# Optimization experiments

Measured on AMD Instinct MI355X. Metric: run time of the kernel, lower is better.

## Reference

```python
import jax, jax.numpy as jnp
import numpy as np


def _gcn(A, x, W, b):
    # GCNConv(improved=True): add_remaining_self_loops(fill=2), symmetric normalization.
    n = A.shape[0]
    idx = jnp.arange(n)
    d = jnp.diagonal(A)
    Ahat = A.at[idx, idx].set(jnp.where(d == 0, 2.0, d))  # keep existing self-loop weights
    dinv = 1.0 / jnp.sqrt(Ahat.sum(axis=1))
    return (Ahat * dinv[:, None] * dinv[None, :]) @ (x @ W) + b


def _augment(A):
    # GraphUNet.augment_adj: add self loops, A @ A (spspmm), remove self loops.
    n = A.shape[0]
    idx = jnp.arange(n)
    A1 = A.at[idx, idx].add(1.0)
    return (A1 @ A1).at[idx, idx].set(0.0)


def _pool(A, x, p, k):
    # TopKPooling with tanh nonlinearity.
    score = jnp.tanh((x @ p) / jnp.linalg.norm(p))
    vals, perm = jax.lax.top_k(score, k)
    return A[perm][:, perm], x[perm] * vals[:, None], perm


def _gat(mask, x, W, a_src, a_dst, b, heads, c, concat):
    # GATConv, eval mode (attention dropout inactive). mask[dst, src] includes self loops.
    n = x.shape[0]
    h = (x @ W).reshape(n, heads, c)
    es = jnp.einsum('shc,hc->sh', h, a_src)
    ed = jnp.einsum('dhc,hc->dh', h, a_dst)
    logits = jax.nn.leaky_relu(ed[:, None, :] + es[None, :, :], 0.2)  # [dst, src, h]
    logits = jnp.where(mask[:, :, None], logits, jnp.finfo(logits.dtype).min)
    alpha = jax.nn.softmax(logits, axis=1)  # softmax over sources per destination
    out = jnp.einsum('dsh,shc->dhc', alpha, h)
    out = out.reshape(n, heads * c) if concat else out.mean(axis=1)
    return out + b


def setup_inputs() -> dict:
    key = jax.random.key(0)
    ks = jax.random.split(key, 34)
    N, E, IN, H, OUT, HEADS = 4096, 65536, 3, 64, 128, 4
    r = lambda k, s: jax.random.normal(k, s, jnp.float32) * 0.1
    inp = {}
    inp['x'] = jax.random.normal(ks[0], (N, IN), jnp.float32)
    inp['edge_index'] = jax.random.randint(ks[1], (2, E), 0, N)
    inp['unet_w0'] = r(ks[2], (IN, H)); inp['unet_b0'] = jnp.zeros((H,), jnp.float32)
    inp['unet_w1'] = r(ks[3], (H, H)); inp['unet_b1'] = jnp.zeros((H,), jnp.float32)
    inp['unet_w2'] = r(ks[4], (H, H)); inp['unet_b2'] = jnp.zeros((H,), jnp.float32)
    inp['unet_w3'] = r(ks[5], (H, H)); inp['unet_b3'] = jnp.zeros((H,), jnp.float32)
    inp['pool_p1'] = r(ks[6], (H,)); inp['pool_p2'] = r(ks[7], (H,)); inp['pool_p3'] = r(ks[8], (H,))
    inp['up_w0'] = r(ks[9], (H, H)); inp['up_b0'] = jnp.zeros((H,), jnp.float32)
    inp['up_w1'] = r(ks[10], (H, H)); inp['up_b1'] = jnp.zeros((H,), jnp.float32)
    inp['up_w2'] = r(ks[11], (H, OUT)); inp['up_b2'] = jnp.zeros((OUT,), jnp.float32)
    inp['ln_g'] = jnp.ones((OUT,), jnp.float32); inp['ln_b'] = jnp.zeros((OUT,), jnp.float32)
    inp['res_w'] = r(ks[12], (OUT, OUT)); inp['res_b'] = jnp.zeros((OUT,), jnp.float32)
    inp['gat1_w'] = r(ks[13], (OUT, HEADS * OUT))
    inp['gat1_asrc'] = r(ks[14], (HEADS, OUT)); inp['gat1_adst'] = r(ks[15], (HEADS, OUT))
    inp['gat1_b'] = jnp.zeros((HEADS * OUT,), jnp.float32)
    inp['gat2_w'] = r(ks[16], (HEADS * OUT, OUT))
    inp['gat2_asrc'] = r(ks[17], (1, OUT)); inp['gat2_adst'] = r(ks[18], (1, OUT))
    inp['gat2_b'] = jnp.zeros((OUT,), jnp.float32)
    return inp


def reference(x, edge_index, unet_w0, unet_b0, unet_w1, unet_b1, unet_w2, unet_b2,
              unet_w3, unet_b3, pool_p1, pool_p2, pool_p3, up_w0, up_b0, up_w1, up_b1,
              up_w2, up_b2, ln_g, ln_b, res_w, res_b, gat1_w, gat1_asrc, gat1_adst,
              gat1_b, gat2_w, gat2_asrc, gat2_adst, gat2_b):
    n0 = x.shape[0]
    # Dense weighted adjacency A[dst, src]; duplicate edges accumulate weight (scatter-add).
    A0 = jnp.zeros((n0, n0), x.dtype).at[edge_index[1], edge_index[0]].add(1.0)
    # ---- GraphUNet down path ----
    x0 = jax.nn.relu(_gcn(A0, x, unet_w0, unet_b0))
    k1 = (n0 + 1) // 2
    A1, h1, perm1 = _pool(_augment(A0), x0, pool_p1, k1)
    x1 = jax.nn.relu(_gcn(A1, h1, unet_w1, unet_b1))
    k2 = (k1 + 1) // 2
    A2, h2, perm2 = _pool(_augment(A1), x1, pool_p2, k2)
    x2 = jax.nn.relu(_gcn(A2, h2, unet_w2, unet_b2))
    k3 = (k2 + 1) // 2
    A3, h3, perm3 = _pool(_augment(A2), x2, pool_p3, k3)
    x3 = jax.nn.relu(_gcn(A3, h3, unet_w3, unet_b3))
    # ---- up path (sum_res=True) ----
    h = x2 + jnp.zeros_like(x2).at[perm3].set(x3)
    h = jax.nn.relu(_gcn(A2, h, up_w0, up_b0))
    h = x1 + jnp.zeros_like(x1).at[perm2].set(h)
    h = jax.nn.relu(_gcn(A1, h, up_w1, up_b1))
    h = x0 + jnp.zeros_like(x0).at[perm1].set(h)
    h = _gcn(A0, h, up_w2, up_b2)  # last up conv: no activation -> [n0, 128]
    # ---- LayerNorm(eps=1e-6) ----
    mu = h.mean(-1, keepdims=True)
    var = ((h - mu) ** 2).mean(-1, keepdims=True)
    u = (h - mu) / jnp.sqrt(var + 1e-6) * ln_g + ln_b
    residual = u @ res_w + res_b
    mask = (A0 > 0) | jnp.eye(n0, dtype=bool)  # GATConv adds self loops
    g = jax.nn.elu(_gat(mask, u, gat1_w, gat1_asrc, gat1_adst, gat1_b, 4, 128, True))
    g = _gat(mask, g, gat2_w, gat2_asrc, gat2_adst, gat2_b, 1, 128, False)
    return g + residual
```

## Files before the change

### kernel.cpp

```cpp
#include <hip/hip_runtime.h>
#include <math.h>


#define TPB 256
#define LDK 88
#define MAXN 128

typedef __attribute__((ext_vector_type(8))) short bf16x8;
typedef __attribute__((ext_vector_type(4))) float f32x4;

__device__ inline ushort f32_to_bf16(float v) {
    unsigned b = __float_as_uint(v);
    return (ushort)((b + 0x7FFF + ((b >> 16) & 1)) >> 16);
}
__device__ inline float bf2f(ushort u) { return __uint_as_float(((unsigned)u) << 16); }

__global__ void bucket_scatter(const int* __restrict__ ei, int E, int* __restrict__ buck,
                               int* __restrict__ cursor) {
    int e = blockIdx.x * TPB + threadIdx.x;
    if (e >= E) return;
    int src = ei[e];
    int dst = ei[E + e];
    int pos = atomicAdd(&cursor[dst], 1);
    if (pos < MAXN) buck[dst * MAXN + pos] = src;
}

__global__ void build_csr(const int* __restrict__ buck, const int* __restrict__ cursor,
                          int n, int* __restrict__ nbr, float* __restrict__ awt,
                          int* __restrict__ acnt, float* __restrict__ dinv,
                          float* __restrict__ selfw) {
    int i = blockIdx.x;
    int tid = threadIdx.x;
    __shared__ int s[MAXN];
    __shared__ int outcnt, selfFound;
    int raw = cursor[i];
    int d = min(raw, MAXN);
    if (tid == 0) { outcnt = 0; selfFound = 0; }
    for (int p = tid; p < d; p += 64) s[p] = buck[i * MAXN + p];
    __syncthreads();
    for (int p = tid; p < d; p += 64)
        if (s[p] == i) atomicOr(&selfFound, 1);
    __syncthreads();
    for (int p = tid; p < d; p += 64) {
        int v = s[p];
        bool first = true;
        for (int q = 0; q < p; ++q)
            if (s[q] == v) { first = false; break; }
        if (first) {
            int w = 1;
            for (int q = p + 1; q < d; ++q) w += (s[q] == v);
            int slot = atomicAdd(&outcnt, 1);
            nbr[i * MAXN + slot] = v;
            awt[i * MAXN + slot] = (float)w + (v == i ? 1.0f : 0.0f);
        }
    }
    __syncthreads();
    if (tid == 0) {
        int cnt = outcnt;
        if (!selfFound && cnt < MAXN) {
            nbr[i * MAXN + cnt] = i;
            awt[i * MAXN + cnt] = 1.0f;
            ++cnt;
        }
        acnt[i] = cnt;
        float sw = selfFound ? 0.f : 2.f;
        dinv[i] = 1.0f / sqrtf((float)raw + sw);
        selfw[i] = sw;
    }
}

__global__ void xw_gemm(const float* __restrict__ xin, const float* __restrict__ W,
                        float* __restrict__ C, int n, int fin, int f) {
    __shared__ float sW[64 * 128];
    int tid = threadIdx.x;
    for (int t = tid; t < fin * f; t += TPB) sW[t] = W[t];
    __syncthreads();
    int rpb = TPB / f;
    int r = blockIdx.x * rpb + tid / f;
    int c = tid - (tid / f) * f;
    if (r >= n) return;
    const float* xr = xin + (size_t)r * fin;
    float acc = 0.f;
    for (int k = 0; k < fin; ++k) acc += xr[k] * sW[k * f + c];
    C[(size_t)r * f + c] = acc;
}

__global__ void spmv_gcn(const int* __restrict__ nbr, const float* __restrict__ awt,
                         const int* __restrict__ acnt, const float* __restrict__ xw,
                         const float* __restrict__ dinv, const float* __restrict__ selfw,
                         const float* __restrict__ bias, float* __restrict__ out,
                         int f, int relu) {
    int i = blockIdx.x;
    int o = threadIdx.x;
    __shared__ int sj[MAXN];
    __shared__ float sw_[MAXN];
    int cnt = acnt[i];
    for (int a = o; a < cnt; a += blockDim.x) {
        sj[a] = nbr[i * MAXN + a];
        sw_[a] = awt[i * MAXN + a];
    }
    __syncthreads();
    if (o >= f) return;
    float sum = 0.f;
    for (int a = 0; a < cnt; ++a) {
        int j = sj[a];
        sum += sw_[a] * (xw[(size_t)j * f + o] * dinv[j]);
    }
    float yi = xw[(size_t)i * f + o] * dinv[i];
    sum -= yi;
    float v = dinv[i] * (sum + selfw[i] * yi) + bias[o];
    if (relu) v = fmaxf(v, 0.f);
    out[(size_t)i * f + o] = v;
}

__global__ void score_kernel2(const float* __restrict__ x, const float* __restrict__ p,
                              float* __restrict__ s, int n) {
    int i = blockIdx.x * TPB + threadIdx.x;
    if (i >= n) return;
    float a = 0.f, nrm = 0.f;
    for (int c = 0; c < 64; ++c) {
        float pc = p[c];
        nrm += pc * pc;
        a += x[(size_t)i * 64 + c] * pc;
    }
    s[i] = tanhf(a / sqrtf(nrm));
}

__global__ void rank_count(const float* __restrict__ s, int n, int* __restrict__ rank) {
    __shared__ float sj[256];
    int i = blockIdx.x * 256 + threadIdx.x;
    int j0 = blockIdx.y * 256;
    sj[threadIdx.x] = s[j0 + threadIdx.x];
    float si = s[i];
    __syncthreads();
    int r = 0;
#pragma unroll 8
    for (int jj = 0; jj < 256; ++jj) {
        float v = sj[jj];
        r += (v > si) || (v == si && (j0 + jj) < i);
    }
    atomicAdd(&rank[i], r);
}

__global__ void scatter_topk_all(const float* __restrict__ s, const int* __restrict__ rank,
                                 int n, int k, int* __restrict__ perm,
                                 float* __restrict__ vals, int* __restrict__ invp) {
    int i = blockIdx.x * TPB + threadIdx.x;
    if (i >= n) return;
    int r = rank[i];
    if (r < k) { perm[r] = i; vals[r] = s[i]; invp[i] = r; }
    else invp[i] = -1;
}

__global__ void gather_feat(const float* __restrict__ x, const int* __restrict__ perm,
                            const float* __restrict__ vals, int k, int f, float* __restrict__ h) {
    int id = blockIdx.x * TPB + threadIdx.x;
    if (id >= k * f) return;
    int r = id / f, c = id - r * f;
    h[id] = x[(size_t)perm[r] * f + c] * vals[r];
}

__global__ void spgemm_aug(const int* __restrict__ nbr, const float* __restrict__ awt,
                           const int* __restrict__ acnt, const int* __restrict__ perm,
                           const int* __restrict__ invp, int k,
                           ushort* __restrict__ Chi, ushort* __restrict__ Clo,
                           float* __restrict__ dinv, float* __restrict__ selfw) {
    __shared__ float row[2048];
    int r = blockIdx.x, tid = threadIdx.x;
    int pi = perm[r];
    for (int j = tid; j < k; j += TPB) row[j] = 0.f;
    __syncthreads();
    int cnt = acnt[pi];
    for (int a = 0; a < cnt; ++a) {
        int t = nbr[pi * MAXN + a];
        float w1 = awt[pi * MAXN + a];
        int c2 = acnt[t];
        for (int b = tid; b < c2; b += TPB) {
            int s = nbr[t * MAXN + b];
            int j = invp[s];
            if (j >= 0) atomicAdd(&row[j], w1 * awt[t * MAXN + b]);
        }
    }
    __syncthreads();
    float psum = 0.f;
    for (int j = tid; j < k; j += TPB) {
        float v = (j == r) ? 0.f : row[j];
        psum += v;
        ushort hi = f32_to_bf16(v);
        size_t o = (size_t)r * k + j;
        Chi[o] = hi;
        Clo[o] = f32_to_bf16(v - bf2f(hi));
    }
    for (int o = 32; o; o >>= 1) psum += __shfl_xor(psum, o);
    __shared__ float sh[4];
    if ((tid & 63) == 0) sh[tid >> 6] = psum;
    __syncthreads();
    if (tid == 0) {
        float tot = sh[0] + sh[1] + sh[2] + sh[3];
        dinv[r] = 1.0f / sqrtf(tot + 2.0f);
        selfw[r] = 2.0f;
    }
}

__global__ void transpose_aug_hl(const ushort* __restrict__ Ahi, const ushort* __restrict__ Alo,
                                 ushort* __restrict__ T, int n) {
    __shared__ float tile[64][65];
    int c0 = blockIdx.x * 64, r0 = blockIdx.y * 64;
    for (int t = threadIdx.x; t < 4096; t += TPB) {
        int r = t >> 6, c = t & 63;
        size_t o = (size_t)(r0 + r) * n + (c0 + c);
        float v = bf2f(Ahi[o]) + bf2f(Alo[o]);
        if (r0 + r == c0 + c) v += 1.0f;
        tile[c][r] = v;
    }
    __syncthreads();
    for (int t = threadIdx.x; t < 4096; t += TPB) {
        int c = t >> 6, r = t & 63;
        T[(size_t)(c0 + c) * n + (r0 + r)] = f32_to_bf16(tile[c][r]);
    }
}

__global__ void gather_rows_aug_hl(const ushort* __restrict__ Ahi, const ushort* __restrict__ Alo,
                                   const int* __restrict__ perm, ushort* __restrict__ Ag,
                                   int n, int rows) {
    int id = blockIdx.x * TPB + threadIdx.x;
    if (id >= rows * n) return;
    int r = id / n, t = id - r * n;
    int pr = perm[r];
    size_t o = (size_t)pr * n + t;
    float v = bf2f(Ahi[o]) + bf2f(Alo[o]);
    if (pr == t) v += 1.0f;
    Ag[id] = f32_to_bf16(v);
}

__global__ void gather_rows_u16(const ushort* __restrict__ T, const int* __restrict__ perm,
                                ushort* __restrict__ Bg, int n, int rows) {
    int id = blockIdx.x * TPB + threadIdx.x;
    if (id >= rows * n) return;
    int r = id / n, t = id - r * n;
    Bg[id] = T[(size_t)perm[r] * n + t];
}

// ... 67 lines not shown
        size_t o = (size_t)r * k + j;
        Chi[o] = hi;
        Clo[o] = f32_to_bf16(v - bf2f(hi));
    }
    for (int o = 32; o; o >>= 1) psum += __shfl_xor(psum, o);
    __shared__ float sh[4];
    if ((tid & 63) == 0) sh[tid >> 6] = psum;
    __syncthreads();
    if (tid == 0) {
        float tot = sh[0] + sh[1] + sh[2] + sh[3];
        dinv[r] = 1.0f / sqrtf(tot + 2.0f);
        selfw[r] = 2.0f;
    }
}

__global__ void __launch_bounds__(256)
gcn_gemm(const ushort* __restrict__ Ahi, const ushort* __restrict__ Alo,
         const ushort* __restrict__ Bhi, const ushort* __restrict__ Blo,
         float* __restrict__ C, int K, int ldc, int kpb) {
    __shared__ __align__(16) ushort sAh[64 * LDK];
    __shared__ __align__(16) ushort sAl[64 * LDK];
    __shared__ __align__(16) ushort sBh[64 * LDK];
    __shared__ __align__(16) ushort sBl[64 * LDK];
    int tid = threadIdx.x;
    int wave = tid >> 6, lane = tid & 63;
    int wr = wave >> 1, wc = wave & 1;
    int m = lane & 15, quad = lane >> 4;
    int i0 = blockIdx.y * 64, j0 = blockIdx.x * 64;
    int kbeg = blockIdx.z * kpb;
    f32x4 acc[2][2];
#pragma unroll
    for (int a = 0; a < 2; ++a)
#pragma unroll
        for (int b = 0; b < 2; ++b) acc[a][b] = (f32x4){0.f, 0.f, 0.f, 0.f};
    for (int k0 = kbeg; k0 < kbeg + kpb; k0 += 64) {
#pragma unroll
        for (int v = 0; v < 2; ++v) {
            int idx = tid + (v << 8);
            int r = idx >> 3, c8 = idx & 7;
            size_t boff = (size_t)(j0 + r) * K + k0 + c8 * 8;
            *(uint4*)&sBh[r * LDK + c8 * 8] = *(const uint4*)&Bhi[boff];
            *(uint4*)&sBl[r * LDK + c8 * 8] = *(const uint4*)&Blo[boff];
            size_t aoff = (size_t)(i0 + r) * K + k0 + c8 * 8;
            *(uint4*)&sAh[r * LDK + c8 * 8] = *(const uint4*)&Ahi[aoff];
            *(uint4*)&sAl[r * LDK + c8 * 8] = *(const uint4*)&Alo[aoff];
        }
        __syncthreads();
#pragma unroll
        for (int kk = 0; kk < 2; ++kk) {
            bf16x8 ah[2], al[2], bh[2], bl[2];
#pragma unroll
            for (int mi = 0; mi < 2; ++mi) {
                ah[mi] = *(const bf16x8*)&sAh[(wr * 32 + mi * 16 + m) * LDK + kk * 32 + quad * 8];
                al[mi] = *(const bf16x8*)&sAl[(wr * 32 + mi * 16 + m) * LDK + kk * 32 + quad * 8];
            }
#pragma unroll
            for (int ni = 0; ni < 2; ++ni) {
                bh[ni] = *(const bf16x8*)&sBh[(wc * 32 + ni * 16 + m) * LDK + kk * 32 + quad * 8];
                bl[ni] = *(const bf16x8*)&sBl[(wc * 32 + ni * 16 + m) * LDK + kk * 32 + quad * 8];
            }
#pragma unroll
            for (int mi = 0; mi < 2; ++mi)
#pragma unroll
                for (int ni = 0; ni < 2; ++ni) {
                    acc[mi][ni] = __builtin_amdgcn_mfma_f32_16x16x32_bf16(ah[mi], bh[ni], acc[mi][ni], 0, 0, 0);
                    acc[mi][ni] = __builtin_amdgcn_mfma_f32_16x16x32_bf16(ah[mi], bl[ni], acc[mi][ni], 0, 0, 0);
                    acc[mi][ni] = __builtin_amdgcn_mfma_f32_16x16x32_bf16(al[mi], bh[ni], acc[mi][ni], 0, 0, 0);
                }
        }
        __syncthreads();
    }
#pragma unroll
    for (int mi = 0; mi < 2; ++mi)
#pragma unroll
        for (int ni = 0; ni < 2; ++ni)
#pragma unroll
            for (int r = 0; r < 4; ++r) {
                int gi = i0 + wr * 32 + mi * 16 + quad * 4 + r;
                int gj = j0 + wc * 32 + ni * 16 + m;
                atomicAdd(&C[(size_t)gi * ldc + gj], acc[mi][ni][r]);
            }
}

__global__ void build_yT_z(const float* __restrict__ xw, const float* __restrict__ dinv,
                           ushort* __restrict__ Bhi, ushort* __restrict__ Blo,
                           float* __restrict__ Cp, int n, int f) {
    __shared__ float t[64][65];
    int k0 = blockIdx.x * 64, c0 = blockIdx.y * 64;
#pragma unroll
    for (int v = 0; v < 16; ++v) {
        int idx = threadIdx.x + v * 256;
        int r = idx >> 6, c = idx & 63;
        t[r][c] = xw[(size_t)(k0 + r) * f + (c0 + c)] * dinv[k0 + r];
        Cp[(size_t)(k0 + r) * f + (c0 + c)] = 0.f;
    }
    __syncthreads();
#pragma unroll
    for (int v = 0; v < 16; ++v) {
        int idx = threadIdx.x + v * 256;
        int c = idx >> 6, k = idx & 63;
        float val = t[k][c];
        ushort hi = f32_to_bf16(val);
        size_t o = (size_t)(c0 + c) * n + (k0 + k);
        Bhi[o] = hi;
        Blo[o] = f32_to_bf16(val - bf2f(hi));
    }
}

__global__ void gcn_epilogue(const float* __restrict__ C, const float* __restrict__ xw,
                             const float* __restrict__ dinv, const float* __restrict__ selfw,
                             const float* __restrict__ b, float* __restrict__ out,
                             int n, int f, int relu) {
    int id = blockIdx.x * TPB + threadIdx.x;
    if (id >= n * f) return;
    int i = id / f, c = id - i * f;
    float y = xw[id] * dinv[i];
    float v = dinv[i] * (C[id] + selfw[i] * y) + b[c];
    if (relu) v = fmaxf(v, 0.f);
    out[id] = v;
}

__global__ void unpool_add(const float* __restrict__ xsrc, const float* __restrict__ h,
                           const int* __restrict__ invp, int n, int f, float* __restrict__ t) {
    int id = blockIdx.x * TPB + threadIdx.x;
    if (id >= n * f) return;
    int i = id / f, c = id - i * f;
    int r = invp[i];
    float v = xsrc[id];
    if (r >= 0) v += h[(size_t)r * f + c];
    t[id] = v;
}

__global__ void layernorm(const float* __restrict__ h, const float* __restrict__ g,
                          const float* __restrict__ b, float* __restrict__ u, int n) {
    int i = blockIdx.x;
    int t = threadIdx.x;
    float v = h[(size_t)i * 128 + t];
    __shared__ float s0[2], s1[2];
    float sum = v;
    for (int o = 32; o; o >>= 1) sum += __shfl_xor(sum, o);
    if ((t & 63) == 0) s0[t >> 6] = sum;
    __syncthreads();
    float mu = (s0[0] + s0[1]) * (1.0f / 128.0f);
    float d = v - mu;
    float sq = d * d;
    for (int o = 32; o; o >>= 1) sq += __shfl_xor(sq, o);
    if ((t & 63) == 0) s1[t >> 6] = sq;
    __syncthreads();
    float var = (s1[0] + s1[1]) * (1.0f / 128.0f);
    u[(size_t)i * 128 + t] = d / sqrtf(var + 1e-6f) * g[t] + b[t];
}

__global__ void transpose_split(const float* __restrict__ W, ushort* __restrict__ Bhi,
                                ushort* __restrict__ Blo, int K, int N) {
    __shared__ float tile[64][65];
    int n0 = blockIdx.x * 64, k0 = blockIdx.y * 64;
    for (int t = threadIdx.x; t < 4096; t += TPB) {
        int r = t >> 6, c = t & 63;
        tile[r][c] = W[(size_t)(k0 + r) * N + (n0 + c)];
    }
    __syncthreads();
    for (int t = threadIdx.x; t < 4096; t += TPB) {
        int c = t >> 6, r = t & 63;
        float v = tile[r][c];
        ushort hi = f32_to_bf16(v);
        size_t o = (size_t)(n0 + c) * K + (k0 + r);
        Bhi[o] = hi;
        Blo[o] = f32_to_bf16(v - bf2f(hi));
    }
}

__global__ void __launch_bounds__(256)
gemm_bt_store(const float* __restrict__ A, const ushort* __restrict__ Bhi,
              const ushort* __restrict__ Blo, const float* __restrict__ bias,
              float* __restrict__ C, int K, int N) {
    __shared__ __align__(16) ushort sAh[64 * LDK];
    __shared__ __align__(16) ushort sAl[64 * LDK];
    __shared__ __align__(16) ushort sBh[64 * LDK];
    __shared__ __align__(16) ushort sBl[64 * LDK];
    int tid = threadIdx.x;
    int wave = tid >> 6, lane = tid & 63;
    int wr = wave >> 1, wc = wave & 1;
    int m = lane & 15, quad = lane >> 4;
    int i0 = blockIdx.y * 64, j0 = blockIdx.x * 64;
    f32x4 acc[2][2];
#pragma unroll
    for (int a = 0; a < 2; ++a)
#pragma unroll
        for (int b = 0; b < 2; ++b) acc[a][b] = (f32x4){0.f, 0.f, 0.f, 0.f};
    for (int k0 = 0; k0 < K; k0 += 64) {
#pragma unroll
        for (int v = 0; v < 2; ++v) {
            int idx = tid + (v << 8);
            int r = idx >> 3, c8 = idx & 7;
            size_t boff = (size_t)(j0 + r) * K + k0 + c8 * 8;
            *(uint4*)&sBh[r * LDK + c8 * 8] = *(const uint4*)&Bhi[boff];
            *(uint4*)&sBl[r * LDK + c8 * 8] = *(const uint4*)&Blo[boff];
            size_t aoff = (size_t)(i0 + r) * K + k0 + c8 * 8;
            float4 fa = *(const float4*)&A[aoff];
            float4 fb = *(const float4*)&A[aoff + 4];
            ushort h0 = f32_to_bf16(fa.x), h1 = f32_to_bf16(fa.y);
            ushort h2 = f32_to_bf16(fa.z), h3 = f32_to_bf16(fa.w);
            ushort h4 = f32_to_bf16(fb.x), h5 = f32_to_bf16(fb.y);
            ushort h6 = f32_to_bf16(fb.z), h7 = f32_to_bf16(fb.w);
            uint4 ph, pl;
            ph.x = (uint)h0 | ((uint)h1 << 16);
            ph.y = (uint)h2 | ((uint)h3 << 16);
            ph.z = (uint)h4 | ((uint)h5 << 16);
            ph.w = (uint)h6 | ((uint)h7 << 16);
            pl.x = (uint)f32_to_bf16(fa.x - bf2f(h0)) | ((uint)f32_to_bf16(fa.y - bf2f(h1)) << 16);
            pl.y = (uint)f32_to_bf16(fa.z - bf2f(h2)) | ((uint)f32_to_bf16(fa.w - bf2f(h3)) << 16);
            pl.z = (uint)f32_to_bf16(fb.x - bf2f(h4)) | ((uint)f32_to_bf16(fb.y - bf2f(h5)) << 16);
            pl.w = (uint)f32_to_bf16(fb.z - bf2f(h6)) | ((uint)f32_to_bf16(fb.w - bf2f(h7)) << 16);
            *(uint4*)&sAh[r * LDK + c8 * 8] = ph;
            *(uint4*)&sAl[r * LDK + c8 * 8] = pl;
        }
        __syncthreads();
#pragma unroll
        for (int kk = 0; kk < 2; ++kk) {
            bf16x8 ah[2], al[2], bh[2], bl[2];
#pragma unroll
            for (int mi = 0; mi < 2; ++mi) {
                ah[mi] = *(const bf16x8*)&sAh[(wr * 32 + mi * 16 + m) * LDK + kk * 32 + quad * 8];
                al[mi] = *(const bf16x8*)&sAl[(wr * 32 + mi * 16 + m) * LDK + kk * 32 + quad * 8];
            }
#pragma unroll
            for (int ni = 0; ni < 2; ++ni) {
                bh[ni] = *(const bf16x8*)&sBh[(wc * 32 + ni * 16 + m) * LDK + kk * 32 + quad * 8];
                bl[ni] = *(const bf16x8*)&sBl[(wc * 32 + ni * 16 + m) * LDK + kk * 32 + quad * 8];
            }
#pragma unroll
            for (int mi = 0; mi < 2; ++mi)
#pragma unroll
                for (int ni = 0; ni < 2; ++ni) {
                    acc[mi][ni] = __builtin_amdgcn_mfma_f32_16x16x32_bf16(ah[mi], bh[ni], acc[mi][ni], 0, 0, 0);
                    acc[mi][ni] = __builtin_amdgcn_mfma_f32_16x16x32_bf16(ah[mi], bl[ni], acc[mi][ni], 0, 0, 0);
                    acc[mi][ni] = __builtin_amdgcn_mfma_f32_16x16x32_bf16(al[mi], bh[ni], acc[mi][ni], 0, 0, 0);
                }
        }
        __syncthreads();
    }
#pragma unroll
// ... 88 lines not shown
#pragma unroll
            for (int r = 0; r < 4; ++r) {
                int gi = i0 + wr * 32 + mi * 16 + quad * 4 + r;
                int gj = j0 + wc * 32 + ni * 16 + m;
                atomicAdd(&C[(size_t)gi * N + gj], acc[mi][ni][r]);
            }
}

__global__ void attn_coef2(const float* __restrict__ hf, const float* __restrict__ asrc,
                           const float* __restrict__ adst, float* __restrict__ es,
                           float* __restrict__ ed, int heads) {
    int j = blockIdx.x;
    int wave = threadIdx.x >> 6, lane = threadIdx.x & 63;
    if (wave >= heads) return;
    const float* hp = hf + (size_t)j * heads * 128 + wave * 128;
    float v0 = hp[lane], v1 = hp[lane + 64];
    float a = v0 * asrc[wave * 128 + lane] + v1 * asrc[wave * 128 + lane + 64];
    float d = v0 * adst[wave * 128 + lane] + v1 * adst[wave * 128 + lane + 64];
    for (int o = 32; o; o >>= 1) { a += __shfl_xor(a, o); d += __shfl_xor(d, o); }
    if (lane == 0) { es[j * heads + wave] = a; ed[j * heads + wave] = d; }
}

__global__ void gat_sparse(const int* __restrict__ nbr, const int* __restrict__ ncnt, int n,
                           const float* __restrict__ hf, const float* __restrict__ es,
                           const float* __restrict__ ed, const float* __restrict__ bias,
                           const float* __restrict__ resid, float* __restrict__ out,
                           int heads, int mode) {
    int i = blockIdx.x;
    int tid = threadIdx.x;
    __shared__ int idx[MAXN];
    __shared__ float lg[MAXN * 4];
    __shared__ float hmax[4], hsum[4];
    int m = ncnt[i];
    for (int t = tid; t < m; t += TPB) idx[t] = nbr[i * MAXN + t];
    __syncthreads();
    for (int t = tid; t < m * heads; t += TPB) {
        int jl = t / heads, h = t - jl * heads;
        float l = ed[i * heads + h] + es[idx[jl] * heads + h];
        lg[jl * heads + h] = (l > 0.f) ? l : 0.2f * l;
    }
    __syncthreads();
    int h = tid >> 6, lane = tid & 63;
    if (h < heads) {
        float mx = -3.4e38f;
        for (int jl = lane; jl < m; jl += 64) mx = fmaxf(mx, lg[jl * heads + h]);
        for (int o = 32; o; o >>= 1) mx = fmaxf(mx, __shfl_xor(mx, o));
        if (lane == 0) hmax[h] = mx;
    }
    __syncthreads();
    if (h < heads) {
        float mx = hmax[h];
        float sm = 0.f;
        for (int jl = lane; jl < m; jl += 64) {
            float p = expf(lg[jl * heads + h] - mx);
            lg[jl * heads + h] = p;
            sm += p;
        }
        for (int o = 32; o; o >>= 1) sm += __shfl_xor(sm, o);
        if (lane == 0) hsum[h] = sm;
    }
    __syncthreads();
    int width = heads * 128;
    for (int o = tid; o < width; o += TPB) {
        int hh = o >> 7;
        float acc = 0.f;
        for (int jl = 0; jl < m; ++jl)
            acc += lg[jl * heads + hh] * hf[(size_t)idx[jl] * width + o];
        float v = acc / hsum[hh] + bias[o];
        if (mode == 0) v = (v > 0.f) ? v : expm1f(v);
        else v += resid[(size_t)i * width + o];
        out[(size_t)i * width + o] = v;
    }
}

static inline int cdiv(int a, int b) { return (a + b - 1) / b; }

static int pick_z(int gx, int gy, int K) {
    int z = 1;
    while (gx * gy * z < 384 && K / (2 * z) >= 64) z <<= 1;
    return z;
}

static void run_gcn_dense(hipStream_t stream, const ushort* Ahi, const ushort* Alo,
                          int n, const float* xin, int fin,
                          const float* W, const float* bias, int f,
                          const float* dinv, const float* selfw,
                          float* xw, ushort* yThi, ushort* yTlo, float* Cp,
                          float* out, int relu) {
    xw_gemm<<<cdiv(n, TPB / f), TPB, 0, stream>>>(xin, W, xw, n, fin, f);
    build_yT_z<<<dim3(n / 64, f / 64), TPB, 0, stream>>>(xw, dinv, yThi, yTlo, Cp, n, f);
    int z = pick_z(f / 64, n / 64, n);
    gcn_gemm<<<dim3(f / 64, n / 64, z), TPB, 0, stream>>>(Ahi, Alo, yThi, yTlo, Cp, n, f, n / z);
    gcn_epilogue<<<cdiv(n * f, TPB), TPB, 0, stream>>>(Cp, xw, dinv, selfw, bias, out, n, f, relu);
}

static void run_gcn_sparse(hipStream_t stream, const int* nbr, const float* awt,
                           const int* acnt, int n, const float* xin, int fin,
                           const float* W, const float* bias, int f,
                           const float* dinv, const float* selfw,
                           float* xw, float* out, int relu) {
    xw_gemm<<<cdiv(n, TPB / f), TPB, 0, stream>>>(xin, W, xw, n, fin, f);
    spmv_gcn<<<n, f, 0, stream>>>(nbr, awt, acnt, xw, dinv, selfw, bias, out, f, relu);
}

static void run_topk(hipStream_t stream, const float* score, int n, int k, int* rank,
                     int* perm, float* vals, int* invp) {
    hipMemsetAsync(rank, 0, n * sizeof(int), stream);
    rank_count<<<dim3(n / 256, n / 256), 256, 0, stream>>>(score, n, rank);
    scatter_topk_all<<<cdiv(n, TPB), TPB, 0, stream>>>(score, rank, n, k, perm, vals, invp);
}

static void run_aug_dense(hipStream_t stream, const ushort* Ahi, const ushort* Alo, int n,
                          const int* perm, int k, ushort* Tbf, ushort* Agb, ushort* Bgb,
                          float* Caug, ushort* Chi, ushort* Clo, float* dinv, float* selfw) {
    transpose_aug_hl<<<dim3(n / 64, n / 64), TPB, 0, stream>>>(Ahi, Alo, Tbf, n);
    gather_rows_aug_hl<<<cdiv(k * n, TPB), TPB, 0, stream>>>(Ahi, Alo, perm, Agb, n, k);
    gather_rows_u16<<<cdiv(k * n, TPB), TPB, 0, stream>>>(Tbf, perm, Bgb, n, k);
    hipMemsetAsync(Caug, 0, (size_t)k * k * sizeof(float), stream);
    int z = 8;
    aug_gemm_acc<<<dim3(k / 64, k / 64, z), TPB, 0, stream>>>(Agb, Bgb, Caug, n, k, n / z);
    aug_finalize<<<k, TPB, 0, stream>>>(Caug, k, Chi, Clo, dinv, selfw);
}

extern "C" void kernel_launch(void* const* d_in, const int* in_sizes, int n_in,
                              void* d_out, int out_size, void* d_ws, size_t ws_size,
                              hipStream_t stream) {
    const float* x   = (const float*)d_in[0];
    const int*   ei  = (const int*)d_in[1];
    const float* w0  = (const float*)d_in[2];  const float* b0  = (const float*)d_in[3];
    const float* w1  = (const float*)d_in[4];  const float* b1  = (const float*)d_in[5];
    const float* w2  = (const float*)d_in[6];  const float* b2  = (const float*)d_in[7];
    const float* w3  = (const float*)d_in[8];  const float* b3  = (const float*)d_in[9];
    const float* p1  = (const float*)d_in[10];
    const float* p2  = (const float*)d_in[11];
    const float* p3  = (const float*)d_in[12];
    const float* uw0 = (const float*)d_in[13]; const float* ub0 = (const float*)d_in[14];
    const float* uw1 = (const float*)d_in[15]; const float* ub1 = (const float*)d_in[16];
    const float* uw2 = (const float*)d_in[17]; const float* ub2 = (const float*)d_in[18];
    const float* lng = (const float*)d_in[19]; const float* lnb = (const float*)d_in[20];
    const float* rw  = (const float*)d_in[21]; const float* rb  = (const float*)d_in[22];
    const float* g1w = (const float*)d_in[23];
    const float* g1as = (const float*)d_in[24]; const float* g1ad = (const float*)d_in[25];
    const float* g1b = (const float*)d_in[26];
    const float* g2w = (const float*)d_in[27];
    const float* g2as = (const float*)d_in[28]; const float* g2ad = (const float*)d_in[29];
    const float* g2b = (const float*)d_in[30];

    const int N = 4096, E = 65536;
    const int K1 = 2048, K2 = 1024, K3 = 512;

    float* base = (float*)d_ws;
    size_t off = 0;
    auto alloc = [&](size_t nf) { float* p = base + off; off += (nf + 63) & ~(size_t)63; return p; };

    ushort* A1hi = (ushort*)alloc((size_t)K1 * K1 / 2);
    ushort* A1lo = (ushort*)alloc((size_t)K1 * K1 / 2);
    ushort* A2hi = (ushort*)alloc((size_t)K2 * K2 / 2);
    ushort* A2lo = (ushort*)alloc((size_t)K2 * K2 / 2);
    ushort* A3hi = (ushort*)alloc((size_t)K3 * K3 / 2);
    ushort* A3lo = (ushort*)alloc((size_t)K3 * K3 / 2);
    ushort* Tbf  = (ushort*)alloc((size_t)K1 * K1 / 2);
    ushort* Agb  = (ushort*)alloc((size_t)K2 * K1 / 2);
    ushort* Bgb  = (ushort*)alloc((size_t)K2 * K1 / 2);
    ushort* yThi = (ushort*)alloc((size_t)128 * N / 2);
    ushort* yTlo = (ushort*)alloc((size_t)128 * N / 2);
    ushort* Whi  = (ushort*)alloc((size_t)512 * 128 / 2);
    ushort* Wlo  = (ushort*)alloc((size_t)512 * 128 / 2);
    float* Caug  = alloc((size_t)K2 * K2);
    float* Cp    = alloc((size_t)N * 128);
    float* x0    = alloc((size_t)N * 64);
    float* x1    = alloc((size_t)K1 * 64);
    float* x2    = alloc((size_t)K2 * 64);
    float* x3    = alloc((size_t)K3 * 64);
    float* h1    = alloc((size_t)K1 * 64);
    float* h2    = alloc((size_t)K2 * 64);
    float* h3    = alloc((size_t)K3 * 64);
    float* xw    = alloc((size_t)N * 128);
    float* dinv0 = alloc(N);  float* selfw0 = alloc(N);
    float* dinv1 = alloc(K1); float* selfw1 = alloc(K1);
    float* dinv2 = alloc(K2); float* selfw2 = alloc(K2);
    float* dinv3 = alloc(K3); float* selfw3 = alloc(K3);
    int*   cursor= (int*)alloc(N);
    int*   buck  = (int*)alloc((size_t)N * MAXN);
    float* score = alloc(N);
    int*   rank  = (int*)alloc(N);
    float* vals1 = alloc(K1); float* vals2 = alloc(K2); float* vals3 = alloc(K3);
    int*   perm1 = (int*)alloc(K1); int* perm2 = (int*)alloc(K2); int* perm3 = (int*)alloc(K3);
    int*   invp1 = (int*)alloc(N);  int* invp2 = (int*)alloc(K1); int* invp3 = (int*)alloc(K2);
    int*   nbr   = (int*)alloc((size_t)N * MAXN);
    float* awt   = alloc((size_t)N * MAXN);
    int*   acnt  = (int*)alloc(N);
    float* t2    = alloc((size_t)K2 * 64);
    float* t1    = alloc((size_t)K1 * 64);
    float* t0    = alloc((size_t)N * 64);
    float* hfin  = alloc((size_t)N * 128);
    float* u     = alloc((size_t)N * 128);
    float* resid = alloc((size_t)N * 128);
    float* hf1   = alloc((size_t)N * 512);
    float* es1   = alloc((size_t)N * 4); float* ed1 = alloc((size_t)N * 4);
    float* g1    = alloc((size_t)N * 512);
    float* hf2   = alloc((size_t)N * 128);
    float* es2   = alloc(N); float* ed2 = alloc(N);
    (void)ws_size; (void)n_in; (void)in_sizes; (void)out_size;

    hipMemsetAsync(cursor, 0, N * sizeof(int), stream);
    bucket_scatter<<<cdiv(E, TPB), TPB, 0, stream>>>(ei, E, buck, cursor);
    build_csr<<<N, 64, 0, stream>>>(buck, cursor, N, nbr, awt, acnt, dinv0, selfw0);

    run_gcn_sparse(stream, nbr, awt, acnt, N, x, 3, w0, b0, 64, dinv0, selfw0, xw, x0, 1);

    score_kernel2<<<cdiv(N, TPB), TPB, 0, stream>>>(x0, p1, score, N);
    run_topk(stream, score, N, K1, rank, perm1, vals1, invp1);
    spgemm_aug<<<K1, TPB, 0, stream>>>(nbr, awt, acnt, perm1, invp1, K1,
                                       A1hi, A1lo, dinv1, selfw1);
    gather_feat<<<cdiv(K1 * 64, TPB), TPB, 0, stream>>>(x0, perm1, vals1, K1, 64, h1);
    run_gcn_dense(stream, A1hi, A1lo, K1, h1, 64, w1, b1, 64,
                  dinv1, selfw1, xw, yThi, yTlo, Cp, x1, 1);

    score_kernel2<<<cdiv(K1, TPB), TPB, 0, stream>>>(x1, p2, score, K1);
    run_topk(stream, score, K1, K2, rank, perm2, vals2, invp2);
    run_aug_dense(stream, A1hi, A1lo, K1, perm2, K2, Tbf, Agb, Bgb, Caug,
                  A2hi, A2lo, dinv2, selfw2);
    gather_feat<<<cdiv(K2 * 64, TPB), TPB, 0, stream>>>(x1, perm2, vals2, K2, 64, h2);
    run_gcn_dense(stream, A2hi, A2lo, K2, h2, 64, w2, b2, 64,
                  dinv2, selfw2, xw, yThi, yTlo, Cp, x2, 1);

    score_kernel2<<<cdiv(K2, TPB), TPB, 0, stream>>>(x2, p3, score, K2);
    run_topk(stream, score, K2, K3, rank, perm3, vals3, invp3);
    run_aug_dense(stream, A2hi, A2lo, K2, perm3, K3, Tbf, Agb, Bgb, Caug,
                  A3hi, A3lo, dinv3, selfw3);
    gather_feat<<<cdiv(K3 * 64, TPB), TPB, 0, stream>>>(x2, perm3, vals3, K3, 64, h3);
    run_gcn_dense(stream, A3hi, A3lo, K3, h3, 64, w3, b3, 64,
                  dinv3, selfw3, xw, yThi, yTlo, Cp, x3, 1);

    unpool_add<<<cdiv(K2 * 64, TPB), TPB, 0, stream>>>(x2, x3, invp3, K2, 64, t2);
    run_gcn_dense(stream, A2hi, A2lo, K2, t2, 64, uw0, ub0, 64,
                  dinv2, selfw2, xw, yThi, yTlo, Cp, h2, 1);

    unpool_add<<<cdiv(K1 * 64, TPB), TPB, 0, stream>>>(x1, h2, invp2, K1, 64, t1);
    run_gcn_dense(stream, A1hi, A1lo, K1, t1, 64, uw1, ub1, 64,
                  dinv1, selfw1, xw, yThi, yTlo, Cp, h1, 1);

    unpool_add<<<cdiv(N * 64, TPB), TPB, 0, stream>>>(x0, h1, invp1, N, 64, t0);
    run_gcn_sparse(stream, nbr, awt, acnt, N, t0, 64, uw2, ub2, 128,
                   dinv0, selfw0, xw, hfin, 0);

    layernorm<<<N, 128, 0, stream>>>(hfin, lng, lnb, u, N);
    transpose_split<<<dim3(2, 2), TPB, 0, stream>>>(rw, Whi, Wlo, 128, 128);
    gemm_bt_store<<<dim3(2, N / 64), TPB, 0, stream>>>(u, Whi, Wlo, rb, resid, 128, 128);

    transpose_split<<<dim3(8, 2), TPB, 0, stream>>>(g1w, Whi, Wlo, 128, 512);
    gemm_bt_store<<<dim3(8, N / 64), TPB, 0, stream>>>(u, Whi, Wlo, nullptr, hf1, 128, 512);
    attn_coef2<<<N, 256, 0, stream>>>(hf1, g1as, g1ad, es1, ed1, 4);
    gat_sparse<<<N, TPB, 0, stream>>>(nbr, acnt, N, hf1, es1, ed1, g1b, nullptr, g1, 4, 0);

    transpose_split<<<dim3(2, 8), TPB, 0, stream>>>(g2w, Whi, Wlo, 512, 128);
    hipMemsetAsync(hf2, 0, (size_t)N * 128 * sizeof(float), stream);
    gemm_bt_split<<<dim3(2, N / 64, 4), TPB, 0, stream>>>(g1, Whi, Wlo, hf2, 512, 128, 128);
    attn_coef2<<<N, 64, 0, stream>>>(hf2, g2as, g2ad, es2, ed2, 1);
    gat_sparse<<<N, TPB, 0, stream>>>(nbr, acnt, N, hf2, es2, ed2, g2b, resid, (float*)d_out, 1, 1);
}
```

Measured before the change: 486.5 us.

## Fuse gather/unpool, x@W and bf16 transpose-split into one GCN prologue kernel

Merges the feature gather (top-k pooling) or unpool-add, the X·W product, and the dinv-scaled bf16 hi/lo transposed split plus Cp zeroing into a single kernel per dense GCN layer. The final sparse GCN input gets the unpool fused into its X·W GEMM. The three weight transpose-splits are batched into one launch at the start. The aim is to remove about a dozen small kernel launches and the intermediate global round trips. The cost is less parallelism per block and narrow 8-byte transposed stores.

```diff
diff --git a/kernel.cpp b/kernel.cpp
--- a/kernel.cpp
+++ b/kernel.cpp
@@ -83,6 +83,75 @@
     float acc = 0.f;
     for (int k = 0; k < fin; ++k) acc += xr[k] * sW[k * f + c];
     C[(size_t)r * f + c] = acc;
+}
+
+__global__ void xw_gemm_unpool(const float* __restrict__ xsrc, const float* __restrict__ hprev,
+                               const int* __restrict__ invp, const float* __restrict__ W,
+                               float* __restrict__ C, int n) {
+    __shared__ float sW[64 * 128];
+    __shared__ float sin_[2][64];
+    int tid = threadIdx.x;
+    for (int t = tid; t < 8192; t += TPB) sW[t] = W[t];
+    int r0 = blockIdx.x * 2;
+    int lr = tid >> 7, c = tid & 127;
+    int r = r0 + lr;
+    if (c < 64) {
+        float v = xsrc[(size_t)r * 64 + c];
+        int q = invp[r];
+        if (q >= 0) v += hprev[(size_t)q * 64 + c];
+        sin_[lr][c] = v;
+    }
+    __syncthreads();
+    float acc = 0.f;
+#pragma unroll
+    for (int k = 0; k < 64; ++k) acc += sin_[lr][k] * sW[k * 128 + c];
+    C[(size_t)r * 128 + c] = acc;
+}
+
+__global__ void fused_in_gemm(const float* __restrict__ xsrc, const int* __restrict__ perm,
+                              const float* __restrict__ vals, const float* __restrict__ hprev,
+                              const int* __restrict__ invp, const float* __restrict__ W,
+                              const float* __restrict__ dinv, float* __restrict__ xw,
+                              ushort* __restrict__ yThi, ushort* __restrict__ yTlo,
+                              float* __restrict__ Cp, int n, int mode) {
+    __shared__ float sW[64 * 64];
+    __shared__ float sin_[4][64];
+    __shared__ float sy[4][64];
+    int tid = threadIdx.x;
+    for (int t = tid; t < 4096; t += TPB) sW[t] = W[t];
+    int r0 = blockIdx.x * 4;
+    int lr = tid >> 6, c = tid & 63;
+    int r = r0 + lr;
+    float v;
+    if (mode == 0) {
+        v = xsrc[(size_t)perm[r] * 64 + c] * vals[r];
+    } else {
+        v = xsrc[(size_t)r * 64 + c];
+        int q = invp[r];
+        if (q >= 0) v += hprev[(size_t)q * 64 + c];
+    }
+    sin_[lr][c] = v;
+    __syncthreads();
+    float acc = 0.f;
+#pragma unroll
+    for (int k = 0; k < 64; ++k) acc += sin_[lr][k] * sW[k * 64 + c];
+    size_t o = (size_t)r * 64 + c;
+    xw[o] = acc;
+    Cp[o] = 0.f;
+    sy[lr][c] = acc * dinv[r];
+    __syncthreads();
+    if (lr == 0) {
+        float y0 = sy[0][c], y1 = sy[1][c], y2 = sy[2][c], y3 = sy[3][c];
+        ushort h0 = f32_to_bf16(y0), h1 = f32_to_bf16(y1);
+        ushort h2 = f32_to_bf16(y2), h3 = f32_to_bf16(y3);
+        uint2 ph, pl;
+        ph.x = (uint)h0 | ((uint)h1 << 16);
+        ph.y = (uint)h2 | ((uint)h3 << 16);
+        pl.x = (uint)f32_to_bf16(y0 - bf2f(h0)) | ((uint)f32_to_bf16(y1 - bf2f(h1)) << 16);
+        pl.y = (uint)f32_to_bf16(y2 - bf2f(h2)) | ((uint)f32_to_bf16(y3 - bf2f(h3)) << 16);
+        *(uint2*)&yThi[(size_t)c * n + r0] = ph;
+        *(uint2*)&yTlo[(size_t)c * n + r0] = pl;
+    }
 }
 
 __global__ void spmv_gcn(const int* __restrict__ nbr, const float* __restrict__ awt,
@@ -150,14 +219,6 @@
     int r = rank[i];
     if (r < k) { perm[r] = i; vals[r] = s[i]; invp[i] = r; }
     else invp[i] = -1;
-}
-
-__global__ void gather_feat(const float* __restrict__ x, const int* __restrict__ perm,
-                            const float* __restrict__ vals, int k, int f, float* __restrict__ h) {
-    int id = blockIdx.x * TPB + threadIdx.x;
-    if (id >= k * f) return;
-    int r = id / f, c = id - r * f;
-    h[id] = x[(size_t)perm[r] * f + c] * vals[r];
 }
 
 __global__ void spgemm_aug(const int* __restrict__ nbr, const float* __restrict__ awt,
@@ -391,31 +452,6 @@
             }
 }
 
-__global__ void build_yT_z(const float* __restrict__ xw, const float* __restrict__ dinv,
-                           ushort* __restrict__ Bhi, ushort* __restrict__ Blo,
-                           float* __restrict__ Cp, int n, int f) {
-    __shared__ float t[64][65];
-    int k0 = blockIdx.x * 64, c0 = blockIdx.y * 64;
-#pragma unroll
-    for (int v = 0; v < 16; ++v) {
-        int idx = threadIdx.x + v * 256;
-        int r = idx >> 6, c = idx & 63;
-        t[r][c] = xw[(size_t)(k0 + r) * f + (c0 + c)] * dinv[k0 + r];
-        Cp[(size_t)(k0 + r) * f + (c0 + c)] = 0.f;
-    }
-    __syncthreads();
-#pragma unroll
-    for (int v = 0; v < 16; ++v) {
-        int idx = threadIdx.x + v * 256;
-        int c = idx >> 6, k = idx & 63;
-        float val = t[k][c];
-        ushort hi = f32_to_bf16(val);
-        size_t o = (size_t)(c0 + c) * n + (k0 + k);
-        Bhi[o] = hi;
-        Blo[o] = f32_to_bf16(val - bf2f(hi));
-    }
-}
-
 __global__ void gcn_epilogue(const float* __restrict__ C, const float* __restrict__ xw,
                              const float* __restrict__ dinv, const float* __restrict__ selfw,
                              const float* __restrict__ b, float* __restrict__ out,
@@ -429,17 +465,6 @@
     out[id] = v;
 }
 
-__global__ void unpool_add(const float* __restrict__ xsrc, const float* __restrict__ h,
-                           const int* __restrict__ invp, int n, int f, float* __restrict__ t) {
-    int id = blockIdx.x * TPB + threadIdx.x;
-    if (id >= n * f) return;
-    int i = id / f, c = id - i * f;
-    int r = invp[i];
-    float v = xsrc[id];
-    if (r >= 0) v += h[(size_t)r * f + c];
-    t[id] = v;
-}
-
 __global__ void layernorm(const float* __restrict__ h, const float* __restrict__ g,
                           const float* __restrict__ b, float* __restrict__ u, int n) {
     int i = blockIdx.x;
@@ -460,13 +485,21 @@
     u[(size_t)i * 128 + t] = d / sqrtf(var + 1e-6f) * g[t] + b[t];
 }
 
-__global__ void transpose_split(const float* __restrict__ W, ushort* __restrict__ Bhi,
-                                ushort* __restrict__ Blo, int K, int N) {
+__global__ void prep_weights(const float* __restrict__ rw, const float* __restrict__ g1w,
+                             const float* __restrict__ g2w,
+                             ushort* __restrict__ W1hi, ushort* __restrict__ W1lo,
+                             ushort* __restrict__ W2hi, ushort* __restrict__ W2lo,
+                             ushort* __restrict__ W3hi, ushort* __restrict__ W3lo) {
     __shared__ float tile[64][65];
-    int n0 = blockIdx.x * 64, k0 = blockIdx.y * 64;
+    int b = blockIdx.x;
+    const float* W; ushort *Bhi, *Blo; int K, Nn, bx, by;
+    if (b < 4)       { W = rw;  Bhi = W1hi; Blo = W1lo; K = 128; Nn = 128; bx = b & 1;        by = b >> 1; }
+    else if (b < 20) { int t = b - 4;  W = g1w; Bhi = W2hi; Blo = W2lo; K = 128; Nn = 512; bx = t & 7; by = t >> 3; }
+    else             { int t = b - 20; W = g2w; Bhi = W3hi; Blo = W3lo; K = 512; Nn = 128; bx = t & 1; by = t >> 1; }
+    int n0 = bx * 64, k0 = by * 64;
     for (int t = threadIdx.x; t < 4096; t += TPB) {
         int r = t >> 6, c = t & 63;
-        tile[r][c] = W[(size_t)(k0 + r) * N + (n0 + c)];
+        tile[r][c] = W[(size_t)(k0 + r) * Nn + (n0 + c)];
     }
     __syncthreads();
     for (int t = threadIdx.x; t < 4096; t += TPB) {
@@ -721,25 +754,17 @@
 }
 
 static void run_gcn_dense(hipStream_t stream, const ushort* Ahi, const ushort* Alo,
-                          int n, const float* xin, int fin,
-                          const float* W, const float* bias, int f,
+                          int n, const float* xsrc, const int* perm, const float* vals,
+                          const float* hprev, const int* invp, int mode,
+                          const float* W, const float* bias,
                           const float* dinv, const float* selfw,
                           float* xw, ushort* yThi, ushort* yTlo, float* Cp,
                           float* out, int relu) {
-    xw_gemm<<<cdiv(n, TPB / f), TPB, 0, stream>>>(xin, W, xw, n, fin, f);
-    build_yT_z<<<dim3(n / 64, f / 64), TPB, 0, stream>>>(xw, dinv, yThi, yTlo, Cp, n, f);
-    int z = pick_z(f / 64, n / 64, n);
-    gcn_gemm<<<dim3(f / 64, n / 64, z), TPB, 0, stream>>>(Ahi, Alo, yThi, yTlo, Cp, n, f, n / z);
-    gcn_epilogue<<<cdiv(n * f, TPB), TPB, 0, stream>>>(Cp, xw, dinv, selfw, bias, out, n, f, relu);
-}
-
-static void run_gcn_sparse(hipStream_t stream, const int* nbr, const float* awt,
-                           const int* acnt, int n, const float* xin, int fin,
-                           const float* W, const float* bias, int f,
-                           const float* dinv, const float* selfw,
-                           float* xw, float* out, int relu) {
-    xw_gemm<<<cdiv(n, TPB / f), TPB, 0, stream>>>(xin, W, xw, n, fin, f);
-    spmv_gcn<<<n, f, 0, stream>>>(nbr, awt, acnt, xw, dinv, selfw, bias, out, f, relu);
+    fused_in_gemm<<<n / 4, TPB, 0, stream>>>(xsrc, perm, vals, hprev, invp, W, dinv,
+                                             xw, yThi, yTlo, Cp, n, mode);
+    int z = pick_z(1, n / 64, n);
+    gcn_gemm<<<dim3(1, n / 64, z), TPB, 0, stream>>>(Ahi, Alo, yThi, yTlo, Cp, n, 64, n / z);
+    gcn_epilogue<<<cdiv(n * 64, TPB), TPB, 0, stream>>>(Cp, xw, dinv, selfw, bias, out, n, 64, relu);
 }
 
 static void run_topk(hipStream_t stream, const float* score, int n, int k, int* rank,
@@ -801,19 +826,22 @@
     ushort* Tbf  = (ushort*)alloc((size_t)K1 * K1 / 2);
     ushort* Agb  = (ushort*)alloc((size_t)K2 * K1 / 2);
     ushort* Bgb  = (ushort*)alloc((size_t)K2 * K1 / 2);
-    ushort* yThi = (ushort*)alloc((size_t)128 * N / 2);
-    ushort* yTlo = (ushort*)alloc((size_t)128 * N / 2);
-    ushort* Whi  = (ushort*)alloc((size_t)512 * 128 / 2);
-    ushort* Wlo  = (ushort*)alloc((size_t)512 * 128 / 2);
+    ushort* yThi = (ushort*)alloc((size_t)64 * N / 2);
+    ushort* yTlo = (ushort*)alloc((size_t)64 * N / 2);
+    ushort* W1hi = (ushort*)alloc((size_t)128 * 128 / 2);
+    ushort* W1lo = (ushort*)alloc((size_t)128 * 128 / 2);
+    ushort* W2hi = (ushort*)alloc((size_t)512 * 128 / 2);
+    ushort* W2lo = (ushort*)alloc((size_t)512 * 128 / 2);
+    ushort* W3hi = (ushort*)alloc((size_t)128 * 512 / 2);
+    ushort* W3lo = (ushort*)alloc((size_t)128 * 512 / 2);
     float* Caug  = alloc((size_t)K2 * K2);
-    float* Cp    = alloc((size_t)N * 128);
+    float* Cp    = alloc((size_t)N * 64);
     float* x0    = alloc((size_t)N * 64);
     float* x1    = alloc((size_t)K1 * 64);
     float* x2    = alloc((size_t)K2 * 64);
     float* x3    = alloc((size_t)K3 * 64);
+    float* h2    = alloc((size_t)K2 * 64);
     float* h1    = alloc((size_t)K1 * 64);
-    float* h2    = alloc((size_t)K2 * 64);
-    float* h3    = alloc((size_t)K3 * 64);
     float* xw    = alloc((size_t)N * 128);
     float* dinv0 = alloc(N);  float* selfw0 = alloc(N);
     float* dinv1 = alloc(K1); float* selfw1 = alloc(K1);
@@ -829,9 +857,6 @@
     int*   nbr   = (int*)alloc((size_t)N * MAXN);
     float* awt   = alloc((size_t)N * MAXN);
     int*   acnt  = (int*)alloc(N);
-    float* t2    = alloc((size_t)K2 * 64);
-    float* t1    = alloc((size_t)K1 * 64);
-    float* t0    = alloc((size_t)N * 64);
     float* hfin  = alloc((size_t)N * 128);
     float* u     = alloc((size_t)N * 128);
     float* resid = alloc((size_t)N * 128);
@@ -842,60 +867,54 @@
     float* es2   = alloc(N); float* ed2 = alloc(N);
     (void)ws_size; (void)n_in; (void)in_sizes; (void)out_size;
 
+    prep_weights<<<36, TPB, 0, stream>>>(rw, g1w, g2w, W1hi, W1lo, W2hi, W2lo, W3hi, W3lo);
+
     hipMemsetAsync(cursor, 0, N * sizeof(int), stream);
     bucket_scatter<<<cdiv(E, TPB), TPB, 0, stream>>>(ei, E, buck, cursor);
     build_csr<<<N, 64, 0, stream>>>(buck, cursor, N, nbr, awt, acnt, dinv0, selfw0);
 
-    run_gcn_sparse(stream, nbr, awt, acnt, N, x, 3, w0, b0, 64, dinv0, selfw0, xw, x0, 1);
+    xw_gemm<<<cdiv(N, TPB / 64), TPB, 0, stream>>>(x, w0, xw, N, 3, 64);
+    spmv_gcn<<<N, 64, 0, stream>>>(nbr, awt, acnt, xw, dinv0, selfw0, b0, x0, 64, 1);
 
     score_kernel2<<<cdiv(N, TPB), TPB, 0, stream>>>(x0, p1, score, N);
     run_topk(stream, score, N, K1, rank, perm1, vals1, invp1);
     spgemm_aug<<<K1, TPB, 0, stream>>>(nbr, awt, acnt, perm1, invp1, K1,
                                        A1hi, A1lo, dinv1, selfw1);
-    gather_feat<<<cdiv(K1 * 64, TPB), TPB, 0, stream>>>(x0, perm1, vals1, K1, 64, h1);
-    run_gcn_dense(stream, A1hi, A1lo, K1, h1, 64, w1, b1, 64,
-                  dinv1, selfw1, xw, yThi, yTlo, Cp, x1, 1);
+    run_gcn_dense(stream, A1hi, A1lo, K1, x0, perm1, vals1, nullptr, nullptr, 0,
+                  w1, b1, dinv1, selfw1, xw, yThi, yTlo, Cp, x1, 1);
 
     score_kernel2<<<cdiv(K1, TPB), TPB, 0, stream>>>(x1, p2, score, K1);
     run_topk(stream, score, K1, K2, rank, perm2, vals2, invp2);
     run_aug_dense(stream, A1hi, A1lo, K1, perm2, K2, Tbf, Agb, Bgb, Caug,
                   A2hi, A2lo, dinv2, selfw2);
-    gather_feat<<<cdiv(K2 * 64, TPB), TPB, 0, stream>>>(x1, perm2, vals2, K2, 64, h2);
-    run_gcn_dense(stream, A2hi, A2lo, K2, h2, 64, w2, b2, 64,
-                  dinv2, selfw2, xw, yThi, yTlo, Cp, x2, 1);
+    run_gcn_dense(stream, A2hi, A2lo, K2, x1, perm2, vals2, nullptr, nullptr, 0,
+                  w2, b2, dinv2, selfw2, xw, yThi, yTlo, Cp, x2, 1);
 
     score_kernel2<<<cdiv(K2, TPB), TPB, 0, stream>>>(x2, p3, score, K2);
     run_topk(stream, score, K2, K3, rank, perm3, vals3, invp3);
     run_aug_dense(stream, A2hi, A2lo, K2, perm3, K3, Tbf, Agb, Bgb, Caug,
                   A3hi, A3lo, dinv3, selfw3);
-    gather_feat<<<cdiv(K3 * 64, TPB), TPB, 0, stream>>>(x2, perm3, vals3, K3, 64, h3);
-    run_gcn_dense(stream, A3hi, A3lo, K3, h3, 64, w3, b3, 64,
-                  dinv3, selfw3, xw, yThi, yTlo, Cp, x3, 1);
-
-    unpool_add<<<cdiv(K2 * 64, TPB), TPB, 0, stream>>>(x2, x3, invp3, K2, 64, t2);
-    run_gcn_dense(stream, A2hi, A2lo, K2, t2, 64, uw0, ub0, 64,
-                  dinv2, selfw2, xw, yThi, yTlo, Cp, h2, 1);
-
-    unpool_add<<<cdiv(K1 * 64, TPB), TPB, 0, stream>>>(x1, h2, invp2, K1, 64, t1);
-    run_gcn_dense(stream, A1hi, A1lo, K1, t1, 64, uw1, ub1, 64,
-                  dinv1, selfw1, xw, yThi, yTlo, Cp, h1, 1);
-
-    unpool_add<<<cdiv(N * 64, TPB), TPB, 0, stream>>>(x0, h1, invp1, N, 64, t0);
-    run_gcn_sparse(stream, nbr, awt, acnt, N, t0, 64, uw2, ub2, 128,
-                   dinv0, selfw0, xw, hfin, 0);
+    run_gcn_dense(stream, A3hi, A3lo, K3, x2, perm3, vals3, nullptr, nullptr, 0,
+                  w3, b3, dinv3, selfw3, xw, yThi, yTlo, Cp, x3, 1);
+
+    run_gcn_dense(stream, A2hi, A2lo, K2, x2, nullptr, nullptr, x3, invp3, 1,
+                  uw0, ub0, dinv2, selfw2, xw, yThi, yTlo, Cp, h2, 1);
+
+    run_gcn_dense(stream, A1hi, A1lo, K1, x1, nullptr, nullptr, h2, invp2, 1,
+                  uw1, ub1, dinv1, selfw1, xw, yThi, yTlo, Cp, h1, 1);
+
+    xw_gemm_unpool<<<N / 2, TPB, 0, stream>>>(x0, h1, invp1, uw2, xw, N);
+    spmv_gcn<<<N, 128, 0, stream>>>(nbr, awt, acnt, xw, dinv0, selfw0, ub2, hfin, 128, 0);
 
     layernorm<<<N, 128, 0, stream>>>(hfin, lng, lnb, u, N);
-    transpose_split<<<dim3(2, 2), TPB, 0, stream>>>(rw, Whi, Wlo, 128, 128);
-    gemm_bt_store<<<dim3(2, N / 64), TPB, 0, stream>>>(u, Whi, Wlo, rb, resid, 128, 128);
-
-    transpose_split<<<dim3(8, 2), TPB, 0, stream>>>(g1w, Whi, Wlo, 128, 512);
-    gemm_bt_store<<<dim3(8, N / 64), TPB, 0, stream>>>(u, Whi, Wlo, nullptr, hf1, 128, 512);
+    gemm_bt_store<<<dim3(2, N / 64), TPB, 0, stream>>>(u, W1hi, W1lo, rb, resid, 128, 128);
+
+    gemm_bt_store<<<dim3(8, N / 64), TPB, 0, stream>>>(u, W2hi, W2lo, nullptr, hf1, 128, 512);
     attn_coef2<<<N, 256, 0, stream>>>(hf1, g1as, g1ad, es1, ed1, 4);
     gat_sparse<<<N, TPB, 0, stream>>>(nbr, acnt, N, hf1, es1, ed1, g1b, nullptr, g1, 4, 0);
 
-    transpose_split<<<dim3(2, 8), TPB, 0, stream>>>(g2w, Whi, Wlo, 512, 128);
     hipMemsetAsync(hf2, 0, (size_t)N * 128 * sizeof(float), stream);
-    gemm_bt_split<<<dim3(2, N / 64, 4), TPB, 0, stream>>>(g1, Whi, Wlo, hf2, 512, 128, 128);
+    gemm_bt_split<<<dim3(2, N / 64, 4), TPB, 0, stream>>>(g1, W3hi, W3lo, hf2, 512, 128, 128);
     attn_coef2<<<N, 64, 0, stream>>>(hf2, g2as, g2ad, es2, ed2, 1);
     gat_sparse<<<N, TPB, 0, stream>>>(nbr, acnt, N, hf2, es2, ed2, g2b, resid, (float*)d_out, 1, 1);
 }
```

After: 457.6 us. -5.9%, faster.
